# Kernel optimization log

Measured on AMD Instinct MI355X. Metric: run time of the kernel, lower is better.

Reference implementation:

```python
import jax, jax.numpy as jnp
import numpy as np

REL, DIM = 8, 256
B, S, T = 8, 512, 512


def setup_inputs() -> dict:
    key = jax.random.key(0)
    k = jax.random.split(key, 8)
    return {
        "src_emb": jax.random.normal(k[0], (B, S, DIM), jnp.float32),
        "tar_emb": jax.random.normal(k[1], (B, T, DIM), jnp.float32),
        "src_mask": jnp.ones((B, S), jnp.float32),
        "tar_mask": jnp.ones((B, T), jnp.float32),
        "mul_score_w": jax.random.normal(k[2], (REL, DIM, DIM), jnp.float32) * 0.05,
        "mul_emb_w": jax.random.normal(k[3], (REL, DIM, DIM), jnp.float32) * 0.05,
        "src_none_node": jax.random.normal(k[4], (DIM,), jnp.float32),
        "tar_none_node": jax.random.normal(k[5], (DIM,), jnp.float32),
    }


def reference(src_emb, tar_emb, src_mask, tar_mask,
              mul_score_w, mul_emb_w, src_none_node, tar_none_node):
    b = src_emb.shape[0]
    dim = src_emb.shape[2]
    rel = mul_score_w.shape[0]
    ones = jnp.ones((b, 1), src_mask.dtype)
    # append learned 'none' node to both src and tar (always unmasked)
    src_mask_ = jnp.concatenate([src_mask, ones], axis=1)            # [b, S+1]
    src_emb_ = jnp.concatenate(
        [src_emb, jnp.broadcast_to(src_none_node[None, None, :], (b, 1, dim))], axis=1)
    tar_mask_ = jnp.concatenate([tar_mask, ones], axis=1)            # [b, T+1]
    tar_emb_ = jnp.concatenate(
        [tar_emb, jnp.broadcast_to(tar_none_node[None, None, :], (b, 1, dim))], axis=1)

    # per-relation projected src: [rel, b, S+1, dim]
    scores = jnp.einsum('bsd,rde->rbse', src_emb_, mul_score_w)
    # relation-wise bilinear scores: [rel, b, S+1, T+1]
    st = jnp.einsum('rbse,bte->rbst', scores, tar_emb_)
    pair_mask = src_mask_[:, :, None] * tar_mask_[:, None, :]        # [b, S+1, T+1]
    st = (st + (1.0 - pair_mask)[None] * (-1e10)) * (1.0 / np.sqrt(dim))
    # softmax over the SRC axis (softmax_src=True)
    w = jax.nn.softmax(st, axis=2)                                   # [rel, b, S+1, T+1]

    # per-relation projected tar: [rel, b, T+1, dim]
    rel_tar = jnp.einsum('btd,rde->rbte', tar_emb_, mul_emb_w)
    # use_tar_node=False: drop appended tar none-node from both factors
    rel_tar = rel_tar[:, :, :-1, :]                                  # [rel, b, T, dim]
    w = w[:, :, :, :-1]                                              # [rel, b, S+1, T]

    # tar_sum=True, use_normalize=False: sum over tar then rel, scaled by 1/sqrt(rel)
    mul_emb = jnp.einsum('rbst,rbtd->bsd', w, rel_tar) * (1.0 / np.sqrt(rel))
    # src_none_node present: drop appended src row
    return mul_emb[:, :-1, :]                                        # [b, S, dim]
```

## Files before the change

kernel.cpp:

```cpp
#include <hip/hip_runtime.h>

#define RELN 8
#define DIMN 256
#define BN_  8
#define SN   512
#define TN   512

typedef __attribute__((ext_vector_type(8))) short bf16x8;
typedef __attribute__((ext_vector_type(4))) short bf16x4;
typedef __attribute__((ext_vector_type(4))) float f32x4;

__device__ __forceinline__ unsigned short f2bf(float f) {
    union { float f; unsigned u; } x; x.f = f;
    return (unsigned short)((x.u + 0x7FFFu + ((x.u >> 16) & 1u)) >> 16);
}

#define TBM 128
#define TBN 128
#define TBK 64
#define BP  132

template<int MODE>
__global__ __launch_bounds__(256, 2)
void gemm_bt(const unsigned short* __restrict__ A,
             const unsigned short* __restrict__ B,
             void* __restrict__ C, int K, int lda, int ldb,
             const float* __restrict__ msrc,
             const float* __restrict__ mtar,
             float* __restrict__ Lsum)
{
    __shared__ unsigned short Sh[2][2][TBM * TBK];
    const int tid  = threadIdx.x;
    const int lane = tid & 63;
    const int wv   = tid >> 6;
    const int wr   = (wv >> 1) * 64;
    const int wc   = (wv & 1) * 64;
    const int m0   = blockIdx.x * TBM;
    const int n0   = blockIdx.y * TBN;
    const int z    = blockIdx.z;

    const unsigned short* Ab = A;
    const unsigned short* Bb = B;
    if (MODE == 1)      { Bb += (size_t)z * DIMN * DIMN; }
    else if (MODE == 2) { Ab += (size_t)z * SN * DIMN; Bb += (size_t)(z & 7) * TN * DIMN; }
    else if (MODE == 3) { Bb += (size_t)z * DIMN * DIMN; }
    else                { Ab += (size_t)z * (BN_*SN) * TN;
                          Bb += ((size_t)z * (BN_*DIMN) + (size_t)(m0 >> 9) * DIMN) * TN; }

    auto stage = [&](int buf, int kt) {
        #pragma unroll
        for (int p = 0; p < 4; ++p) {
            int idx8 = p * 256 + tid;
            int row  = idx8 >> 3;
            int col  = (idx8 & 7) << 3;
            __builtin_amdgcn_global_load_lds(
                (const __attribute__((address_space(1))) unsigned int*)
                    &Ab[(size_t)(m0 + row)*lda + kt + col],
                (__attribute__((address_space(3))) unsigned int*)
                    &Sh[buf][0][p*2048 + wv*512], 16, 0, 0);
            __builtin_amdgcn_global_load_lds(
                (const __attribute__((address_space(1))) unsigned int*)
                    &Bb[(size_t)(n0 + row)*ldb + kt + col],
                (__attribute__((address_space(3))) unsigned int*)
                    &Sh[buf][1][p*2048 + wv*512], 16, 0, 0);
        }
    };

    f32x4 acc[4][4] = {};
    const int nsteps = K / TBK;
    stage(0, 0);
    int cur = 0;
    for (int s = 0; s < nsteps; ++s) {
        __syncthreads();
        if (s + 1 < nsteps) stage(cur ^ 1, (s + 1) * TBK);
        const unsigned short* As = Sh[cur][0];
        const unsigned short* Bs = Sh[cur][1];
        #pragma unroll
        for (int kk = 0; kk < 2; ++kk) {
            const int ko = kk*32 + (lane >> 4) * 8;
            bf16x8 af[4], bfv[4];
            #pragma unroll
            for (int i = 0; i < 4; ++i)
                af[i] = *(const bf16x8*)&As[(wr + i*16 + (lane & 15))*TBK + ko];
            #pragma unroll
            for (int j = 0; j < 4; ++j)
                bfv[j] = *(const bf16x8*)&Bs[(wc + j*16 + (lane & 15))*TBK + ko];
            #pragma unroll
            for (int i = 0; i < 4; ++i) {
                #pragma unroll
                for (int j = 0; j < 4; ++j)
                    acc[i][j] = __builtin_amdgcn_mfma_f32_16x16x32_bf16(af[i], bfv[j], acc[i][j], 0, 0, 0);
            }
        }
        cur ^= 1;
    }

    const int r0 = (lane >> 4) * 4;
    const int cl = lane & 15;
    unsigned short* tile = &Sh[0][0][0];

    if (MODE == 2) {
        unsigned short* Cp = (unsigned short*)C + (size_t)z * SN * TN;
        const int b = z & 7;
        float tm[4];
        #pragma unroll
        for (int j = 0; j < 4; ++j) tm[j] = mtar[b*TN + n0 + wc + j*16 + cl];
        float colsum[4] = {0.f, 0.f, 0.f, 0.f};
        __syncthreads();
        #pragma unroll
        for (int i = 0; i < 4; ++i) {
            int rowl = wr + i*16 + r0;
            float sm[4];
            #pragma unroll
            for (int q = 0; q < 4; ++q) sm[q] = msrc[b*SN + m0 + rowl + q];
            #pragma unroll
            for (int j = 0; j < 4; ++j) {
                int coll = wc + j*16 + cl;
                #pragma unroll
                for (int q = 0; q < 4; ++q) {
                    float v = (acc[i][j][q] + (1.f - sm[q]*tm[j]) * -1e10f) * 0.0625f;
                    float e = __expf(v);
                    tile[(rowl + q)*BP + coll] = f2bf(e);
                    colsum[j] += e;
                }
            }
        }
        #pragma unroll
        for (int j = 0; j < 4; ++j) {
            float v = colsum[j];
            v += __shfl_xor(v, 16, 64);
            v += __shfl_xor(v, 32, 64);
            if (lane < 16)
                atomicAdd(&Lsum[(size_t)z*TN + n0 + wc + j*16 + cl], v);
        }
        __syncthreads();
        #pragma unroll
        for (int p = 0; p < 8; ++p) {
            int chunk = p * 256 + tid;
            int row = chunk >> 4, col = (chunk & 15) * 8;
            bf16x8 v = *(const bf16x8*)&tile[row*BP + col];
            *(bf16x8*)&Cp[(size_t)(m0 + row)*TN + n0 + col] = v;
        }
    } else if (MODE == 1) {
        unsigned short* Cp = (unsigned short*)C + (size_t)z * (BN_*SN) * DIMN;
        __syncthreads();
        #pragma unroll
        for (int i = 0; i < 4; ++i) {
            int rowl = wr + i*16 + r0;
            #pragma unroll
            for (int j = 0; j < 4; ++j) {
                int coll = wc + j*16 + cl;
                #pragma unroll
                for (int q = 0; q < 4; ++q)
                    tile[(rowl + q)*BP + coll] = f2bf(acc[i][j][q]);
            }
        }
        __syncthreads();
        #pragma unroll
        for (int p = 0; p < 8; ++p) {
            int chunk = p * 256 + tid;
            int row = chunk >> 4, col = (chunk & 15) * 8;
            bf16x8 v = *(const bf16x8*)&tile[row*BP + col];
            *(bf16x8*)&Cp[(size_t)(m0 + row)*DIMN + n0 + col] = v;
        }
    } else if (MODE == 3) {
        unsigned short* Cp = (unsigned short*)C;
        #pragma unroll
        for (int i = 0; i < 4; ++i) {
            int mrow = m0 + wr + i*16 + r0;
            int b = mrow >> 9, t = mrow & 511;
            float4 Lv = *(const float4*)&Lsum[((size_t)(z*BN_ + b))*TN + t];
            float inv0 = 1.f / Lv.x, inv1 = 1.f / Lv.y,
                  inv2 = 1.f / Lv.z, inv3 = 1.f / Lv.w;
            #pragma unroll
            for (int j = 0; j < 4; ++j) {
                int e = n0 + wc + j*16 + cl;
                bf16x4 v;
                v[0] = (short)f2bf(acc[i][j][0] * inv0);
                v[1] = (short)f2bf(acc[i][j][1] * inv1);
                v[2] = (short)f2bf(acc[i][j][2] * inv2);
                v[3] = (short)f2bf(acc[i][j][3] * inv3);
                *(bf16x4*)&Cp[((size_t)(z*BN_ + b)*DIMN + e)*TN + t] = v;
            }
        }
    } else {
        float* Cp = (float*)C + (size_t)z * (BN_*SN) * DIMN;
        #pragma unroll
        for (int i = 0; i < 4; ++i) {
            int row = m0 + wr + i*16 + r0;
            #pragma unroll
            for (int j = 0; j < 4; ++j) {
                int col = n0 + wc + j*16 + cl;
                #pragma unroll
                for (int q = 0; q < 4; ++q)
                    Cp[(size_t)(row + q)*DIMN + col] = acc[i][j][q];
            }
        }
    }
}

__global__ void reduce8_kernel(const float* __restrict__ part,
                               float* __restrict__ out, int n4)
{
    int i = blockIdx.x * 256 + threadIdx.x;
    if (i < n4) {
        float4 s = {0.f, 0.f, 0.f, 0.f};
        #pragma unroll
        for (int r = 0; r < 8; ++r) {
            float4 v = *(const float4*)&part[(size_t)r*(BN_*SN*DIMN) + i*4];
            s.x += v.x; s.y += v.y; s.z += v.z; s.w += v.w;
        }
        const float k = 0.35355339059327373f;
        float4 o = {s.x*k, s.y*k, s.z*k, s.w*k};
        *(float4*)&out[i*4] = o;
    }
}

__global__ void cvt_bf16_kernel(const float* __restrict__ in,
                                unsigned short* __restrict__ out, int n4)
{
    int i = (blockIdx.x * 256 + threadIdx.x) * 4;
    if (i < n4) {
        float4 v = *(const float4*)(in + i);
        bf16x4 o;
        o[0] = (short)f2bf(v.x); o[1] = (short)f2bf(v.y);
        o[2] = (short)f2bf(v.z); o[3] = (short)f2bf(v.w);
        *(bf16x4*)(out + i) = o;
    }
}

__global__ void wtrans_kernel(const float* __restrict__ w,
                              unsigned short* __restrict__ wt)
{
    __shared__ float tile[32][33];
    int r = blockIdx.z;
    int e0 = blockIdx.x * 32, d0 = blockIdx.y * 32;
    int tx = threadIdx.x & 31, ty = threadIdx.x >> 5;
    #pragma unroll
    for (int k = 0; k < 32; k += 8)
        tile[ty + k][tx] = w[((size_t)r*DIMN + d0 + ty + k)*DIMN + e0 + tx];
    __syncthreads();
    #pragma unroll
    for (int k = 0; k < 32; k += 8)
        wt[((size_t)r*DIMN + e0 + ty + k)*DIMN + d0 + tx] = f2bf(tile[tx][ty + k]);
}

__global__ void scores_none_kernel(const float* __restrict__ w,
                                   const float* __restrict__ none,
                                   float* __restrict__ out)
{
    int r = blockIdx.x, e = threadIdx.x;
    float acc = 0.f;
    for (int d = 0; d < DIMN; ++d)
        acc += none[d] * w[((size_t)r*DIMN + d)*DIMN + e];
    out[r*DIMN + e] = acc;
}

__global__ void initL_kernel(const float* __restrict__ sc_none,
                             const float* __restrict__ tar_emb,
                             const float* __restrict__ tar_mask,
                             float* __restrict__ L)
{
    __shared__ float sn[DIMN];
    __shared__ float part[256];
    int rb = blockIdx.x, r = rb >> 3, b = rb & 7;
    int tl = threadIdx.x & 127, half = threadIdx.x >> 7;
    int t = blockIdx.y * 128 + tl;
    sn[threadIdx.x] = sc_none[r*DIMN + threadIdx.x];
    __syncthreads();
    const float4* row = (const float4*)(tar_emb + ((size_t)b*TN + t)*DIMN + half*128);
    float acc = 0.f;
    #pragma unroll
    for (int k = 0; k < 32; ++k) {
        float4 v = row[k];
        int e = half*128 + k*4;
        acc += v.x*sn[e] + v.y*sn[e+1] + v.z*sn[e+2] + v.w*sn[e+3];
    }
    part[threadIdx.x] = acc;
    __syncthreads();
    if (half == 0) {
        float s = part[tl] + part[tl + 128];
        float tm = tar_mask[b*TN + t];
        L[(size_t)rb*TN + t] = __expf((s + (1.f - tm) * -1e10f) * 0.0625f);
    }
}

extern "C" void kernel_launch(void* const* d_in, const int* in_sizes, int n_in,
                              void* d_out, int out_size, void* d_ws, size_t ws_size,
                              hipStream_t stream)
{
    const float* src_emb  = (const float*)d_in[0];
    const float* tar_emb  = (const float*)d_in[1];
    const float* src_mask = (const float*)d_in[2];
    const float* tar_mask = (const float*)d_in[3];
    const float* w_score  = (const float*)d_in[4];
    const float* w_emb    = (const float*)d_in[5];
    const float* src_none = (const float*)d_in[6];

    size_t off = 0;
    auto alloc = [&](size_t bytes) {
        char* q = (char*)d_ws + off;
        off += (bytes + 255) & ~(size_t)255;
        return q;
    };
    unsigned short* src_bf  = (unsigned short*)alloc((size_t)BN_*SN*DIMN*2);
    unsigned short* tar_bf  = (unsigned short*)alloc((size_t)BN_*TN*DIMN*2);
    unsigned short* wscT    = (unsigned short*)alloc((size_t)RELN*DIMN*DIMN*2);
    unsigned short* wembT   = (unsigned short*)alloc((size_t)RELN*DIMN*DIMN*2);
    unsigned short* scores  = (unsigned short*)alloc((size_t)RELN*BN_*SN*DIMN*2);
    unsigned short* wbuf    = (unsigned short*)alloc((size_t)RELN*BN_*SN*TN*2);
    unsigned short* relT    = (unsigned short*)alloc((size_t)RELN*BN_*DIMN*TN*2);
    float*          outp    = (float*)alloc((size_t)RELN*BN_*SN*DIMN*4);
    float*          sc_none = (float*)alloc((size_t)RELN*DIMN*4);
    float*          Lsum    = (float*)alloc((size_t)RELN*BN_*TN*4);
    if (off > ws_size) return;

    cvt_bf16_kernel<<<1024, 256, 0, stream>>>(src_emb, src_bf, BN_*SN*DIMN);
    cvt_bf16_kernel<<<1024, 256, 0, stream>>>(tar_emb, tar_bf, BN_*TN*DIMN);
    wtrans_kernel<<<dim3(8,8,8), 256, 0, stream>>>(w_score, wscT);
    wtrans_kernel<<<dim3(8,8,8), 256, 0, stream>>>(w_emb,  wembT);
    scores_none_kernel<<<RELN, 256, 0, stream>>>(w_score, src_none, sc_none);
    initL_kernel<<<dim3(64, 4), 256, 0, stream>>>(sc_none, tar_emb, tar_mask, Lsum);

    gemm_bt<1><<<dim3(32, 2, 8), 256, 0, stream>>>(src_bf, wscT, scores, DIMN, DIMN, DIMN,
                                                   nullptr, nullptr, nullptr);
    gemm_bt<2><<<dim3(4, 4, 64), 256, 0, stream>>>(scores, tar_bf, wbuf, DIMN, DIMN, DIMN,
                                                   src_mask, tar_mask, Lsum);
    gemm_bt<3><<<dim3(32, 2, 8), 256, 0, stream>>>(tar_bf, wembT, relT, DIMN, DIMN, DIMN,
                                                   nullptr, nullptr, Lsum);
    gemm_bt<4><<<dim3(32, 2, 8), 256, 0, stream>>>(wbuf, relT, outp, TN, TN, TN,
                                                   nullptr, nullptr, nullptr);
    reduce8_kernel<<<1024, 256, 0, stream>>>(outp, (float*)d_out, BN_*SN*DIMN/4);
}
```

Baseline: 105.0 us.

## Fold relation pairs into final GEMM K-loop and merge preprocessing kernels

The final weighted-sum GEMM now runs four z-slices, each summing two relations along an extended K of 1024, with addressing computed per K tile. This halves the fp32 partial-output buffer and the work of the reduction kernel. The two conversion kernels and the two weight-transpose kernels are each merged into one launch, and the none-node score projection is folded into initL, which now reads bf16 target embeddings. The result is fewer launches and less partial-sum traffic, at the cost of less z-parallelism in the last GEMM, redundant none-node projection per block, and slightly lower precision in the L initialization.

```diff
diff --git a/kernel.cpp b/kernel.cpp
--- a/kernel.cpp
+++ b/kernel.cpp
@@ -13,6 +13,9 @@
 __device__ __forceinline__ unsigned short f2bf(float f) {
     union { float f; unsigned u; } x; x.f = f;
     return (unsigned short)((x.u + 0x7FFFu + ((x.u >> 16) & 1u)) >> 16);
+}
+__device__ __forceinline__ float bf2f(unsigned short h) {
+    union { unsigned u; float f; } x; x.u = (unsigned)h << 16; return x.f;
 }
 
 #define TBM 128
@@ -38,14 +41,14 @@
     const int m0   = blockIdx.x * TBM;
     const int n0   = blockIdx.y * TBN;
     const int z    = blockIdx.z;
+    const int bblk = m0 >> 9;
+    const int rz   = z * 2;
 
     const unsigned short* Ab = A;
     const unsigned short* Bb = B;
     if (MODE == 1)      { Bb += (size_t)z * DIMN * DIMN; }
     else if (MODE == 2) { Ab += (size_t)z * SN * DIMN; Bb += (size_t)(z & 7) * TN * DIMN; }
     else if (MODE == 3) { Bb += (size_t)z * DIMN * DIMN; }
-    else                { Ab += (size_t)z * (BN_*SN) * TN;
-                          Bb += ((size_t)z * (BN_*DIMN) + (size_t)(m0 >> 9) * DIMN) * TN; }
 
     auto stage = [&](int buf, int kt) {
         #pragma unroll
@@ -53,14 +56,22 @@
             int idx8 = p * 256 + tid;
             int row  = idx8 >> 3;
             int col  = (idx8 & 7) << 3;
+            size_t aoff, boff;
+            if (MODE == 4) {
+                int r = rz + (kt >> 9);
+                int t = (kt & 511) + col;
+                aoff = ((size_t)((r*BN_ + bblk)*SN + ((m0 + row) & 511)))*TN + t;
+                boff = ((size_t)((r*BN_ + bblk)*DIMN + (n0 + row)))*TN + t;
+            } else {
+                aoff = (size_t)(m0 + row)*lda + kt + col;
+                boff = (size_t)(n0 + row)*ldb + kt + col;
+            }
             __builtin_amdgcn_global_load_lds(
-                (const __attribute__((address_space(1))) unsigned int*)
-                    &Ab[(size_t)(m0 + row)*lda + kt + col],
+                (const __attribute__((address_space(1))) unsigned int*)&Ab[aoff],
                 (__attribute__((address_space(3))) unsigned int*)
                     &Sh[buf][0][p*2048 + wv*512], 16, 0, 0);
             __builtin_amdgcn_global_load_lds(
-                (const __attribute__((address_space(1))) unsigned int*)
-                    &Bb[(size_t)(n0 + row)*ldb + kt + col],
+                (const __attribute__((address_space(1))) unsigned int*)&Bb[boff],
                 (__attribute__((address_space(3))) unsigned int*)
                     &Sh[buf][1][p*2048 + wv*512], 16, 0, 0);
         }
@@ -199,14 +210,14 @@
     }
 }
 
-__global__ void reduce8_kernel(const float* __restrict__ part,
+__global__ void reduce4_kernel(const float* __restrict__ part,
                                float* __restrict__ out, int n4)
 {
     int i = blockIdx.x * 256 + threadIdx.x;
     if (i < n4) {
         float4 s = {0.f, 0.f, 0.f, 0.f};
         #pragma unroll
-        for (int r = 0; r < 8; ++r) {
+        for (int r = 0; r < 4; ++r) {
             float4 v = *(const float4*)&part[(size_t)r*(BN_*SN*DIMN) + i*4];
             s.x += v.x; s.y += v.y; s.z += v.z; s.w += v.w;
         }
@@ -216,24 +227,31 @@
     }
 }
 
-__global__ void cvt_bf16_kernel(const float* __restrict__ in,
-                                unsigned short* __restrict__ out, int n4)
-{
-    int i = (blockIdx.x * 256 + threadIdx.x) * 4;
-    if (i < n4) {
-        float4 v = *(const float4*)(in + i);
-        bf16x4 o;
-        o[0] = (short)f2bf(v.x); o[1] = (short)f2bf(v.y);
-        o[2] = (short)f2bf(v.z); o[3] = (short)f2bf(v.w);
-        *(bf16x4*)(out + i) = o;
-    }
-}
-
-__global__ void wtrans_kernel(const float* __restrict__ w,
-                              unsigned short* __restrict__ wt)
+__global__ void cvt2_kernel(const float* __restrict__ src,
+                            const float* __restrict__ tar,
+                            unsigned short* __restrict__ src_bf,
+                            unsigned short* __restrict__ tar_bf)
+{
+    int bid = blockIdx.x;
+    const float* in = (bid < 1024) ? src : tar;
+    unsigned short* out = (bid < 1024) ? src_bf : tar_bf;
+    int i = ((bid & 1023) * 256 + threadIdx.x) * 4;
+    float4 v = *(const float4*)(in + i);
+    bf16x4 o;
+    o[0] = (short)f2bf(v.x); o[1] = (short)f2bf(v.y);
+    o[2] = (short)f2bf(v.z); o[3] = (short)f2bf(v.w);
+    *(bf16x4*)(out + i) = o;
+}
+
+__global__ void wtrans2_kernel(const float* __restrict__ wsc,
+                               const float* __restrict__ wem,
+                               unsigned short* __restrict__ wscT,
+                               unsigned short* __restrict__ wembT)
 {
     __shared__ float tile[32][33];
-    int r = blockIdx.z;
+    int r = blockIdx.z & 7;
+    const float* w = (blockIdx.z < 8) ? wsc : wem;
+    unsigned short* wt = (blockIdx.z < 8) ? wscT : wembT;
     int e0 = blockIdx.x * 32, d0 = blockIdx.y * 32;
     int tx = threadIdx.x & 31, ty = threadIdx.x >> 5;
     #pragma unroll
@@ -245,36 +263,33 @@
         wt[((size_t)r*DIMN + e0 + ty + k)*DIMN + d0 + tx] = f2bf(tile[tx][ty + k]);
 }
 
-__global__ void scores_none_kernel(const float* __restrict__ w,
-                                   const float* __restrict__ none,
-                                   float* __restrict__ out)
-{
-    int r = blockIdx.x, e = threadIdx.x;
-    float acc = 0.f;
-    for (int d = 0; d < DIMN; ++d)
-        acc += none[d] * w[((size_t)r*DIMN + d)*DIMN + e];
-    out[r*DIMN + e] = acc;
-}
-
-__global__ void initL_kernel(const float* __restrict__ sc_none,
-                             const float* __restrict__ tar_emb,
+__global__ void initL_kernel(const float* __restrict__ wsc,
+                             const float* __restrict__ none,
+                             const unsigned short* __restrict__ tar_bf,
                              const float* __restrict__ tar_mask,
                              float* __restrict__ L)
 {
     __shared__ float sn[DIMN];
     __shared__ float part[256];
     int rb = blockIdx.x, r = rb >> 3, b = rb & 7;
+    {
+        int e = threadIdx.x;
+        float acc = 0.f;
+        for (int d = 0; d < DIMN; ++d)
+            acc += none[d] * wsc[((size_t)r*DIMN + d)*DIMN + e];
+        sn[e] = acc;
+    }
+    __syncthreads();
     int tl = threadIdx.x & 127, half = threadIdx.x >> 7;
     int t = blockIdx.y * 128 + tl;
-    sn[threadIdx.x] = sc_none[r*DIMN + threadIdx.x];
-    __syncthreads();
-    const float4* row = (const float4*)(tar_emb + ((size_t)b*TN + t)*DIMN + half*128);
+    const unsigned short* rowp = tar_bf + ((size_t)b*TN + t)*DIMN + half*128;
     float acc = 0.f;
     #pragma unroll
-    for (int k = 0; k < 32; ++k) {
-        float4 v = row[k];
-        int e = half*128 + k*4;
-        acc += v.x*sn[e] + v.y*sn[e+1] + v.z*sn[e+2] + v.w*sn[e+3];
+    for (int k = 0; k < 16; ++k) {
+        bf16x8 v = *(const bf16x8*)&rowp[k*8];
+        #pragma unroll
+        for (int j = 0; j < 8; ++j)
+            acc += bf2f((unsigned short)v[j]) * sn[half*128 + k*8 + j];
     }
     part[threadIdx.x] = acc;
     __syncthreads();
@@ -310,25 +325,21 @@
     unsigned short* scores  = (unsigned short*)alloc((size_t)RELN*BN_*SN*DIMN*2);
     unsigned short* wbuf    = (unsigned short*)alloc((size_t)RELN*BN_*SN*TN*2);
     unsigned short* relT    = (unsigned short*)alloc((size_t)RELN*BN_*DIMN*TN*2);
-    float*          outp    = (float*)alloc((size_t)RELN*BN_*SN*DIMN*4);
-    float*          sc_none = (float*)alloc((size_t)RELN*DIMN*4);
+    float*          outp4   = (float*)alloc((size_t)4*BN_*SN*DIMN*4);
     float*          Lsum    = (float*)alloc((size_t)RELN*BN_*TN*4);
     if (off > ws_size) return;
 
-    cvt_bf16_kernel<<<1024, 256, 0, stream>>>(src_emb, src_bf, BN_*SN*DIMN);
-    cvt_bf16_kernel<<<1024, 256, 0, stream>>>(tar_emb, tar_bf, BN_*TN*DIMN);
-    wtrans_kernel<<<dim3(8,8,8), 256, 0, stream>>>(w_score, wscT);
-    wtrans_kernel<<<dim3(8,8,8), 256, 0, stream>>>(w_emb,  wembT);
-    scores_none_kernel<<<RELN, 256, 0, stream>>>(w_score, src_none, sc_none);
-    initL_kernel<<<dim3(64, 4), 256, 0, stream>>>(sc_none, tar_emb, tar_mask, Lsum);
-
+    cvt2_kernel<<<2048, 256, 0, stream>>>(src_emb, tar_emb, src_bf, tar_bf);
+    wtrans2_kernel<<<dim3(8,8,16), 256, 0, stream>>>(w_score, w_emb, wscT, wembT);
+    initL_kernel<<<dim3(64, 4), 256, 0, stream>>>(w_score, src_none, tar_bf,
+                                                  tar_mask, Lsum);
     gemm_bt<1><<<dim3(32, 2, 8), 256, 0, stream>>>(src_bf, wscT, scores, DIMN, DIMN, DIMN,
                                                    nullptr, nullptr, nullptr);
     gemm_bt<2><<<dim3(4, 4, 64), 256, 0, stream>>>(scores, tar_bf, wbuf, DIMN, DIMN, DIMN,
                                                    src_mask, tar_mask, Lsum);
     gemm_bt<3><<<dim3(32, 2, 8), 256, 0, stream>>>(tar_bf, wembT, relT, DIMN, DIMN, DIMN,
                                                    nullptr, nullptr, Lsum);
-    gemm_bt<4><<<dim3(32, 2, 8), 256, 0, stream>>>(wbuf, relT, outp, TN, TN, TN,
+    gemm_bt<4><<<dim3(32, 2, 4), 256, 0, stream>>>(wbuf, relT, outp4, 1024, 0, 0,
                                                    nullptr, nullptr, nullptr);
-    reduce8_kernel<<<1024, 256, 0, stream>>>(outp, (float*)d_out, BN_*SN*DIMN/4);
-}
+    reduce4_kernel<<<1024, 256, 0, stream>>>(outp4, (float*)d_out, BN_*SN*DIMN/4);
+}
```

Result: faster. 94.59 us (-9.9%).
